# Kernel optimization log

Measured on AMD Instinct MI355X. Metric: run time of the kernel, lower is better.

Reference implementation:

```python
import jax, jax.numpy as jnp
import numpy as np

B, T = 48, 88200          # batch of 2 s clips at internal_sr=44100
N_EXC, N_LOOP = 6, 2      # exc_order+1, loop_order+1


def invert_lpc(y, A):
    """x[t] = y[t] + sum_{k=1..N} A[:, t, k-1] * y[t-k]  (zi = 0).
    y: (B,T), A: (B,T,N) -> (B,T). Vectorized time-varying FIR."""
    Bs, Ts = y.shape
    N = A.shape[2]
    yp = jnp.pad(y, ((0, 0), (N, 0)))  # N leading zeros = zero initial state
    # shifts[:, t, k-1] = y[t-k]
    shifts = jnp.stack([yp[:, N - k:N - k + Ts] for k in range(1, N + 1)], axis=2)
    return y + jnp.sum(A * shifts, axis=2)


def sample_wise_lpc(x, A):
    """Time-varying all-pole IIR: y[t] = x[t] - sum_{k=1..N} A[:, t, k-1]*y[t-k].
    Sequential recurrence over T via lax.scan. x: (B,T), A: (B,T,N)."""
    Bs, Ts = x.shape
    N = A.shape[2]

    def step(carry, inp):
        # carry: (B,N) = [y[t-1], ..., y[t-N]]
        xt, at = inp  # (B,), (B,N)
        yt = xt - jnp.sum(at * carry, axis=1)
        new_carry = jnp.concatenate([yt[:, None], carry[:, :-1]], axis=1)
        return new_carry, yt

    carry0 = jnp.zeros((Bs, N), x.dtype)
    _, ys = jax.lax.scan(step, carry0, (x.T, jnp.swapaxes(A, 0, 1)))
    return ys.T  # (B,T)


def setup_inputs() -> dict:
    key = jax.random.key(0)
    k1, k2, k3 = jax.random.split(key, 3)
    y = jax.random.normal(k1, (B, T), dtype=jnp.float32)
    # excitation (FIR-inverse) coefficients: mild, zero-centered
    A_exc = (jax.random.uniform(k2, (B, T, N_EXC), dtype=jnp.float32) - 0.5) * 0.2
    # loop (all-pole) coefficients kept small so the IIR recurrence is stable
    A_loop = (jax.random.uniform(k3, (B, T, N_LOOP), dtype=jnp.float32) - 0.5) * 0.5
    return {"y": y, "A_exc": A_exc, "A_loop": A_loop}


def reference(y, A_exc, A_loop):
    # Core DiffKS pipeline kernel: inverse LPC (feed-forward comb/loop inversion)
    # followed by the sample-wise recursive LPC resynthesis (Karplus-Strong loop).
    x = invert_lpc(y, A_exc)
    return sample_wise_lpc(x, A_loop)
```

## Files before the change

### kernel.cpp

```cpp
#include <hip/hip_runtime.h>


#define T_LEN 88200
#define B_N   48
#define OUT_W 224
#define WUP   32
#define NCH   394
#define WPB   4

__device__ __forceinline__ float4 zero4() { return make_float4(0.f, 0.f, 0.f, 0.f); }

__device__ __forceinline__ float4 ld_guard(const float* p, int t) {
    if (t >= 0 && t + 3 < T_LEN) return *(const float4*)(p + t);
    return zero4();
}

__global__ __launch_bounds__(256, 5) void diffks_kernel(
    const float* __restrict__ y, const float* __restrict__ A_exc,
    const float* __restrict__ A_loop, float* __restrict__ out) {
    const int tid  = threadIdx.x;
    const int widx = tid >> 6;
    const int lane = tid & 63;
    const int w = blockIdx.x * WPB + widx;
    const int b = w / NCH;
    const int c = w - b * NCH;
    const int s  = c * OUT_W;
    const int w0 = s - WUP;
    const int t0 = w0 + 4 * lane;

    const float* yb  = y      + (size_t)b * T_LEN;
    const float* aeb = A_exc  + (size_t)b * T_LEN * 6;
    const float* alb = A_loop + (size_t)b * T_LEN * 2;
    float*       ob  = out    + (size_t)b * T_LEN;

    const bool valid = (t0 >= 0) && (t0 + 3 < T_LEN);
    float4 yv, ae0, ae1, ae2, ae3, ae4, ae5, al0, al1;
    if (valid) {
        yv = *(const float4*)(yb + t0);
        const float4* pae = (const float4*)(aeb + (size_t)t0 * 6);
        ae0 = pae[0]; ae1 = pae[1]; ae2 = pae[2];
        ae3 = pae[3]; ae4 = pae[4]; ae5 = pae[5];
        const float4* pal = (const float4*)(alb + (size_t)t0 * 2);
        al0 = pal[0]; al1 = pal[1];
    } else {
        yv = ae0 = ae1 = ae2 = ae3 = ae4 = ae5 = al0 = al1 = zero4();
    }

    float4 ymid, ylo;
    ymid.x = __shfl_up(yv.x, 1, 64); ymid.y = __shfl_up(yv.y, 1, 64);
    ymid.z = __shfl_up(yv.z, 1, 64); ymid.w = __shfl_up(yv.w, 1, 64);
    ylo.x  = __shfl_up(yv.x, 2, 64); ylo.y  = __shfl_up(yv.y, 2, 64);
    ylo.z  = __shfl_up(yv.z, 2, 64); ylo.w  = __shfl_up(yv.w, 2, 64);
    if (lane == 0) ymid = ld_guard(yb, t0 - 4);
    if (lane <= 1) ylo  = ld_guard(yb, t0 - 8);

    float yw[12] = { ylo.x, ylo.y, ylo.z, ylo.w,
                     ymid.x, ymid.y, ymid.z, ymid.w,
                     yv.x, yv.y, yv.z, yv.w };
    float aef[24] = { ae0.x, ae0.y, ae0.z, ae0.w, ae1.x, ae1.y, ae1.z, ae1.w,
                      ae2.x, ae2.y, ae2.z, ae2.w, ae3.x, ae3.y, ae3.z, ae3.w,
                      ae4.x, ae4.y, ae4.z, ae4.w, ae5.x, ae5.y, ae5.z, ae5.w };
    float alf[8]  = { al0.x, al0.y, al0.z, al0.w, al1.x, al1.y, al1.z, al1.w };

    float xs[4], a1s[4], a2s[4];
    float p00 = 1.f, p01 = 0.f, p10 = 0.f, p11 = 1.f, c0 = 0.f, c1 = 0.f;
#pragma unroll
    for (int j = 0; j < 4; ++j) {
        float xv = yw[8 + j];
#pragma unroll
        for (int k = 1; k <= 6; ++k)
            xv = fmaf(aef[j * 6 + (k - 1)], yw[8 + j - k], xv);
        xs[j] = xv;
        const float a1 = alf[j * 2], a2 = alf[j * 2 + 1];
        a1s[j] = a1; a2s[j] = a2;
        const float n00 = fmaf(-a1, p00, -a2 * p10);
        const float n01 = fmaf(-a1, p01, -a2 * p11);
        p10 = p00; p11 = p01; p00 = n00; p01 = n01;
        const float nc0 = fmaf(-a1, c0, fmaf(-a2, c1, xv));
        c1 = c0; c0 = nc0;
    }

#pragma unroll
    for (int d = 1; d <= 4; d <<= 1) {
        const float q00 = __shfl_up(p00, d, 64), q01 = __shfl_up(p01, d, 64);
        const float q10 = __shfl_up(p10, d, 64), q11 = __shfl_up(p11, d, 64);
        const float qc0 = __shfl_up(c0, d, 64),  qc1 = __shfl_up(c1, d, 64);
        if (lane >= d) {
            const float m00 = fmaf(p00, q00, p01 * q10);
            const float m01 = fmaf(p00, q01, p01 * q11);
            const float m10 = fmaf(p10, q00, p11 * q10);
            const float m11 = fmaf(p10, q01, p11 * q11);
            const float nc0 = fmaf(p00, qc0, fmaf(p01, qc1, c0));
            const float nc1 = fmaf(p10, qc0, fmaf(p11, qc1, c1));
            p00 = m00; p01 = m01; p10 = m10; p11 = m11; c0 = nc0; c1 = nc1;
        }
    }
    {
        const float qc0 = __shfl_up(c0, 8, 64), qc1 = __shfl_up(c1, 8, 64);
        if (lane >= 8) {
            const float nc0 = fmaf(p00, qc0, fmaf(p01, qc1, c0));
            const float nc1 = fmaf(p10, qc0, fmaf(p11, qc1, c1));
            c0 = nc0; c1 = nc1;
        }
    }

    float y1 = __shfl_up(c0, 1, 64);
    float y2 = __shfl_up(c1, 1, 64);
    if (lane == 0) { y1 = 0.f; y2 = 0.f; }
    float ov[4];
#pragma unroll
    for (int j = 0; j < 4; ++j) {
        const float yt = fmaf(-a1s[j], y1, fmaf(-a2s[j], y2, xs[j]));
        y2 = y1; y1 = yt;
        ov[j] = yt;
    }

    if (lane >= 8 && t0 < T_LEN)
        *(float4*)(ob + t0) = make_float4(ov[0], ov[1], ov[2], ov[3]);
}

extern "C" void kernel_launch(void* const* d_in, const int* in_sizes, int n_in,
                              void* d_out, int out_size, void* d_ws, size_t ws_size,
                              hipStream_t stream) {
    const float* y      = (const float*)d_in[0];
    const float* A_exc  = (const float*)d_in[1];
    const float* A_loop = (const float*)d_in[2];
    float* out = (float*)d_out;

    const int waves = B_N * NCH;
    const int grid  = waves / WPB;
    diffks_kernel<<<grid, 256, 0, stream>>>(y, A_exc, A_loop, out);
}
```

Measured before the change: 187.8 us.

## Process eight samples per lane to halve warm-up overhead and widen loads

Each lane now handles eight consecutive samples instead of four, so a wave covers 480 outputs with the same 32-sample warm-up. That reduces the fraction of redundantly loaded and recomputed data. The prefix scan over the 2x2 transfer matrices needs one fewer shuffle step. Blocks grow to 512 threads with 8 waves each. The trade-off is higher register pressure per thread, which may lower occupancy.

```diff
diff --git a/kernel.cpp b/kernel.cpp
--- a/kernel.cpp
+++ b/kernel.cpp
@@ -3,10 +3,12 @@
 
 #define T_LEN 88200
 #define B_N   48
-#define OUT_W 224
+#define SPL   8
+#define OUT_W 480
 #define WUP   32
-#define NCH   394
-#define WPB   4
+#define NCH   184
+#define WPB   8
+#define NWAVES (B_N * NCH)
 
 __device__ __forceinline__ float4 zero4() { return make_float4(0.f, 0.f, 0.f, 0.f); }
 
@@ -15,7 +17,7 @@
     return zero4();
 }
 
-__global__ __launch_bounds__(256, 5) void diffks_kernel(
+__global__ __launch_bounds__(512, 4) void diffks_kernel(
     const float* __restrict__ y, const float* __restrict__ A_exc,
     const float* __restrict__ A_loop, float* __restrict__ out) {
     const int tid  = threadIdx.x;
@@ -26,53 +28,66 @@
     const int c = w - b * NCH;
     const int s  = c * OUT_W;
     const int w0 = s - WUP;
-    const int t0 = w0 + 4 * lane;
+    const int t0 = w0 + SPL * lane;
 
     const float* yb  = y      + (size_t)b * T_LEN;
     const float* aeb = A_exc  + (size_t)b * T_LEN * 6;
     const float* alb = A_loop + (size_t)b * T_LEN * 2;
     float*       ob  = out    + (size_t)b * T_LEN;
 
-    const bool valid = (t0 >= 0) && (t0 + 3 < T_LEN);
-    float4 yv, ae0, ae1, ae2, ae3, ae4, ae5, al0, al1;
+    const bool valid = (t0 >= 0) && (t0 < T_LEN);
+    float4 yv0, yv1, ae[12], al[4];
     if (valid) {
-        yv = *(const float4*)(yb + t0);
+        yv0 = *(const float4*)(yb + t0);
+        yv1 = *(const float4*)(yb + t0 + 4);
         const float4* pae = (const float4*)(aeb + (size_t)t0 * 6);
-        ae0 = pae[0]; ae1 = pae[1]; ae2 = pae[2];
-        ae3 = pae[3]; ae4 = pae[4]; ae5 = pae[5];
+#pragma unroll
+        for (int k = 0; k < 12; ++k) ae[k] = pae[k];
         const float4* pal = (const float4*)(alb + (size_t)t0 * 2);
-        al0 = pal[0]; al1 = pal[1];
+#pragma unroll
+        for (int k = 0; k < 4; ++k) al[k] = pal[k];
     } else {
-        yv = ae0 = ae1 = ae2 = ae3 = ae4 = ae5 = al0 = al1 = zero4();
+        yv0 = yv1 = zero4();
+#pragma unroll
+        for (int k = 0; k < 12; ++k) ae[k] = zero4();
+#pragma unroll
+        for (int k = 0; k < 4; ++k) al[k] = zero4();
     }
 
-    float4 ymid, ylo;
-    ymid.x = __shfl_up(yv.x, 1, 64); ymid.y = __shfl_up(yv.y, 1, 64);
-    ymid.z = __shfl_up(yv.z, 1, 64); ymid.w = __shfl_up(yv.w, 1, 64);
-    ylo.x  = __shfl_up(yv.x, 2, 64); ylo.y  = __shfl_up(yv.y, 2, 64);
-    ylo.z  = __shfl_up(yv.z, 2, 64); ylo.w  = __shfl_up(yv.w, 2, 64);
-    if (lane == 0) ymid = ld_guard(yb, t0 - 4);
-    if (lane <= 1) ylo  = ld_guard(yb, t0 - 8);
+    float4 pv0, pv1;
+    pv0.x = __shfl_up(yv0.x, 1, 64); pv0.y = __shfl_up(yv0.y, 1, 64);
+    pv0.z = __shfl_up(yv0.z, 1, 64); pv0.w = __shfl_up(yv0.w, 1, 64);
+    pv1.x = __shfl_up(yv1.x, 1, 64); pv1.y = __shfl_up(yv1.y, 1, 64);
+    pv1.z = __shfl_up(yv1.z, 1, 64); pv1.w = __shfl_up(yv1.w, 1, 64);
+    if (lane == 0) {
+        pv0 = ld_guard(yb, t0 - 8);
+        pv1 = ld_guard(yb, t0 - 4);
+    }
 
-    float yw[12] = { ylo.x, ylo.y, ylo.z, ylo.w,
-                     ymid.x, ymid.y, ymid.z, ymid.w,
-                     yv.x, yv.y, yv.z, yv.w };
-    float aef[24] = { ae0.x, ae0.y, ae0.z, ae0.w, ae1.x, ae1.y, ae1.z, ae1.w,
-                      ae2.x, ae2.y, ae2.z, ae2.w, ae3.x, ae3.y, ae3.z, ae3.w,
-                      ae4.x, ae4.y, ae4.z, ae4.w, ae5.x, ae5.y, ae5.z, ae5.w };
-    float alf[8]  = { al0.x, al0.y, al0.z, al0.w, al1.x, al1.y, al1.z, al1.w };
+    float yw[16] = { pv0.x, pv0.y, pv0.z, pv0.w, pv1.x, pv1.y, pv1.z, pv1.w,
+                     yv0.x, yv0.y, yv0.z, yv0.w, yv1.x, yv1.y, yv1.z, yv1.w };
+    float aef[48] = {
+        ae[0].x, ae[0].y, ae[0].z, ae[0].w, ae[1].x, ae[1].y, ae[1].z, ae[1].w,
+        ae[2].x, ae[2].y, ae[2].z, ae[2].w, ae[3].x, ae[3].y, ae[3].z, ae[3].w,
+        ae[4].x, ae[4].y, ae[4].z, ae[4].w, ae[5].x, ae[5].y, ae[5].z, ae[5].w,
+        ae[6].x, ae[6].y, ae[6].z, ae[6].w, ae[7].x, ae[7].y, ae[7].z, ae[7].w,
+        ae[8].x, ae[8].y, ae[8].z, ae[8].w, ae[9].x, ae[9].y, ae[9].z, ae[9].w,
+        ae[10].x, ae[10].y, ae[10].z, ae[10].w, ae[11].x, ae[11].y, ae[11].z, ae[11].w };
+    float alf[16] = { al[0].x, al[0].y, al[0].z, al[0].w,
+                      al[1].x, al[1].y, al[1].z, al[1].w,
+                      al[2].x, al[2].y, al[2].z, al[2].w,
+                      al[3].x, al[3].y, al[3].z, al[3].w };
 
-    float xs[4], a1s[4], a2s[4];
+    float xs[SPL];
     float p00 = 1.f, p01 = 0.f, p10 = 0.f, p11 = 1.f, c0 = 0.f, c1 = 0.f;
 #pragma unroll
-    for (int j = 0; j < 4; ++j) {
+    for (int j = 0; j < SPL; ++j) {
         float xv = yw[8 + j];
 #pragma unroll
         for (int k = 1; k <= 6; ++k)
             xv = fmaf(aef[j * 6 + (k - 1)], yw[8 + j - k], xv);
         xs[j] = xv;
-        const float a1 = alf[j * 2], a2 = alf[j * 2 + 1];
-        a1s[j] = a1; a2s[j] = a2;
+        const float a1 = alf[2 * j], a2 = alf[2 * j + 1];
         const float n00 = fmaf(-a1, p00, -a2 * p10);
         const float n01 = fmaf(-a1, p01, -a2 * p11);
         p10 = p00; p11 = p01; p00 = n00; p01 = n01;
@@ -81,7 +96,7 @@
     }
 
 #pragma unroll
-    for (int d = 1; d <= 4; d <<= 1) {
+    for (int d = 1; d <= 2; d <<= 1) {
         const float q00 = __shfl_up(p00, d, 64), q01 = __shfl_up(p01, d, 64);
         const float q10 = __shfl_up(p10, d, 64), q11 = __shfl_up(p11, d, 64);
         const float qc0 = __shfl_up(c0, d, 64),  qc1 = __shfl_up(c1, d, 64);
@@ -96,8 +111,8 @@
         }
     }
     {
-        const float qc0 = __shfl_up(c0, 8, 64), qc1 = __shfl_up(c1, 8, 64);
-        if (lane >= 8) {
+        const float qc0 = __shfl_up(c0, 4, 64), qc1 = __shfl_up(c1, 4, 64);
+        if (lane >= 4) {
             const float nc0 = fmaf(p00, qc0, fmaf(p01, qc1, c0));
             const float nc1 = fmaf(p10, qc0, fmaf(p11, qc1, c1));
             c0 = nc0; c1 = nc1;
@@ -107,16 +122,17 @@
     float y1 = __shfl_up(c0, 1, 64);
     float y2 = __shfl_up(c1, 1, 64);
     if (lane == 0) { y1 = 0.f; y2 = 0.f; }
-    float ov[4];
 #pragma unroll
-    for (int j = 0; j < 4; ++j) {
-        const float yt = fmaf(-a1s[j], y1, fmaf(-a2s[j], y2, xs[j]));
+    for (int j = 0; j < SPL; ++j) {
+        const float yt = fmaf(-alf[2 * j], y1, fmaf(-alf[2 * j + 1], y2, xs[j]));
         y2 = y1; y1 = yt;
-        ov[j] = yt;
+        xs[j] = yt;
     }
 
-    if (lane >= 8 && t0 < T_LEN)
-        *(float4*)(ob + t0) = make_float4(ov[0], ov[1], ov[2], ov[3]);
+    if (lane >= 4 && t0 < T_LEN) {
+        *(float4*)(ob + t0)     = make_float4(xs[0], xs[1], xs[2], xs[3]);
+        *(float4*)(ob + t0 + 4) = make_float4(xs[4], xs[5], xs[6], xs[7]);
+    }
 }
 
 extern "C" void kernel_launch(void* const* d_in, const int* in_sizes, int n_in,
@@ -127,7 +143,6 @@
     const float* A_loop = (const float*)d_in[2];
     float* out = (float*)d_out;
 
-    const int waves = B_N * NCH;
-    const int grid  = waves / WPB;
-    diffks_kernel<<<grid, 256, 0, stream>>>(y, A_exc, A_loop, out);
+    const int grid = NWAVES / WPB;
+    diffks_kernel<<<grid, 512, 0, stream>>>(y, A_exc, A_loop, out);
 }
```

After: 198.3 us. 5.6% more time.
